# Kernel tuning notes

Hardware: AMD Instinct MI355X
Metric: run time of the kernel (lower is better)

Reference implementation:

```python
import math
import jax, jax.numpy as jnp
import numpy as np

B, T, D, K, R, KC = 4, 2048, 1024, 8, 16, 4
H = 4 * D  # mlp hidden


def setup_inputs() -> dict:
    key = jax.random.key(0)
    ks = jax.random.split(key, 12)
    s = lambda i, shape: jax.random.normal(ks[i], shape, jnp.float32) * 0.02
    # state_decay_logit init: geometric decays in [dmin, dmax], logit = log(p) - log1p(-p)
    dmin, dmax = 0.9, 0.999
    dec = np.exp(np.linspace(math.log(dmin), math.log(dmax), K))
    decay_logit = jnp.asarray(np.log(dec) - np.log1p(-dec), jnp.float32)
    return dict(
        x=jax.random.normal(ks[0], (B, T, D), jnp.float32),
        conv_w=s(1, (D, 1, KC)),            # depthwise conv kernel (torch Conv1d weight)
        gp_w=s(2, (D, D)), gp_b=jnp.zeros((D,), jnp.float32),
        up_w=s(3, (D, H)), up_b=jnp.zeros((H,), jnp.float32),
        dn_w=s(4, (H, D)), dn_b=jnp.zeros((D,), jnp.float32),
        si_w=s(5, (D, K * D)),              # state_in (no bias)
        so_w=s(6, (K * D, D)),              # state_out (no bias)
        decay_logit=decay_logit,
        rs_w=s(7, (D, R)), rs_b=jnp.zeros((R,), jnp.float32),
        rwg_w=s(8, (D, 1)), rwg_b=jnp.zeros((1,), jnp.float32),
        rv_w=s(9, (D, D)), rv_b=jnp.zeros((D,), jnp.float32),
        gr_w=s(10, (D, 1)), gr_b=jnp.zeros((1,), jnp.float32),
        gl_w=s(11, (D, 1)), gl_b=jnp.zeros((1,), jnp.float32),
    )


def _rms_norm(x, eps=1e-6):
    return x * jax.lax.rsqrt(jnp.mean(x * x, axis=-1, keepdims=True) + eps)


def _forward(x, conv_w, gp_w, gp_b, up_w, up_b, dn_w, dn_b, si_w, so_w,
             decay_logit, rs_w, rs_b, rwg_w, rwg_b, rv_w, rv_b, gr_w, gr_b, gl_w, gl_b):
    Bx, Tx, Dx = x.shape
    u = _rms_norm(x)
    # --- local mixer: causal depthwise conv + sigmoid gate + SiLU MLP ---
    xc = jax.lax.conv_general_dilated(
        jnp.swapaxes(u, 1, 2), conv_w, window_strides=(1,),
        padding=[(KC - 1, 0)], feature_group_count=Dx,
        dimension_numbers=('NCH', 'OIH', 'NCH'))
    xc = jnp.swapaxes(xc, 1, 2)                       # (B,T,D) causal conv output
    xg = xc * jax.nn.sigmoid(xc @ gp_w + gp_b)
    local = jax.nn.silu(xg @ up_w + up_b) @ dn_w + dn_b
    # --- per-channel exponential-decay state + register read/write scan ---
    dec = jax.nn.sigmoid(decay_logit)                 # (K,)
    z = (u @ si_w).reshape(Bx, Tx, K, Dx)             # state_in, (B,T,K,D)
    sel = jax.nn.softmax(u @ rs_w + rs_b, axis=-1)    # soft register address (B,T,R)
    wg = jax.nn.sigmoid(u @ rwg_w + rwg_b)            # write gate (B,T,1)
    v = u @ rv_w + rv_b                                # register value (B,T,D)

    def step(carry, inp):
        s, regs = carry
        z_t, sel_t, w_t, v_t = inp
        read = jnp.einsum('br,brd->bd', sel_t, regs)  # soft read before write
        ws = (w_t * sel_t)[:, :, None]                # (B,R,1)
        regs = regs * (1.0 - ws) + ws * v_t[:, None, :]
        s = dec[None, :, None] * s + z_t
        return (s, regs), (s, read)

    init = (jnp.zeros((Bx, K, Dx), x.dtype), jnp.zeros((Bx, R, Dx), x.dtype))
    tm = lambda a: jnp.swapaxes(a, 0, 1)              # time-major for scan
    _, (s_all, reads) = jax.lax.scan(step, init, (tm(z), tm(sel), tm(wg), tm(v)))
    s_all = tm(s_all)                                 # (B,T,K,D)
    reads = tm(reads)                                 # (B,T,D)
    long_out = jnp.einsum('btkd,kde->bte', s_all, so_w.reshape(K, Dx, Dx))
    g_long = jax.nn.sigmoid(u @ gl_w + gl_b)
    g_reg = jax.nn.sigmoid(u @ gr_w + gr_b)
    return x + local + g_long * long_out + g_reg * reads


def reference(x, conv_w, gp_w, gp_b, up_w, up_b, dn_w, dn_b, si_w, so_w,
              decay_logit, rs_w, rs_b, rwg_w, rwg_b, rv_w, rv_b, gr_w, gr_b, gl_w, gl_b):
    return _forward(x, conv_w, gp_w, gp_b, up_w, up_b, dn_w, dn_b, si_w, so_w,
                    decay_logit, rs_w, rs_b, rwg_w, rwg_b, rv_w, rv_b, gr_w, gr_b, gl_w, gl_b)
```

## Files before the change

kernel.cpp:

```cpp
#include <hip/hip_runtime.h>

typedef unsigned short u16;
typedef __bf16 bf16x8 __attribute__((ext_vector_type(8)));
typedef float f32x4 __attribute__((ext_vector_type(4)));
typedef u16 u16x4 __attribute__((ext_vector_type(4)));

#define D_ 1024
#define T_ 2048
#define B_ 4
#define K_ 8
#define R_ 16
#define H_ 4096
#define NROW (B_*T_)
#define CH 32
#define CL (T_/CH)
#define CHS 64
#define CLS (T_/CHS)

__device__ __forceinline__ u16 f2bf(float f){
  union{float f;unsigned u;} v; v.f=f;
  unsigned r = v.u + 0x7FFFu + ((v.u>>16)&1u);
  return (u16)(r>>16);
}
__device__ __forceinline__ float bf2f(u16 b){
  union{unsigned u;float f;} v; v.u = ((unsigned)b)<<16; return v.f;
}
__device__ __forceinline__ float sigm(float x){ return 1.f/(1.f+__expf(-x)); }

__device__ __forceinline__ void gload_lds16(const void* g, void* l){
  __builtin_amdgcn_global_load_lds((const __attribute__((address_space(1))) void*)g,
                                   (__attribute__((address_space(3))) void*)l, 16, 0, 0);
}

__global__ __launch_bounds__(256) void fill_k(float* __restrict__ out, long n, float v){
  long i = (long)blockIdx.x*256 + threadIdx.x;
  if (i < n) out[i] = v;
}

__global__ __launch_bounds__(256) void transpose_cast(const float* __restrict__ in, u16* __restrict__ out,
                                                      int R, int C){
  __shared__ float tile[32][33];
  int bx = blockIdx.x*32;
  int by = blockIdx.y*32;
  int tx = threadIdx.x & 31, ty = threadIdx.x >> 5;
  #pragma unroll
  for (int i=0;i<32;i+=8) tile[ty+i][tx] = in[(size_t)(by+ty+i)*C + bx+tx];
  __syncthreads();
  #pragma unroll
  for (int i=0;i<32;i+=8) out[(size_t)(bx+ty+i)*R + by+tx] = f2bf(tile[tx][ty+i]);
}

__global__ __launch_bounds__(256) void castbf(const float* __restrict__ in, u16* __restrict__ out, long n){
  long i = (long)blockIdx.x*256 + threadIdx.x;
  if (i < n) out[i] = f2bf(in[i]);
}

__global__ __launch_bounds__(256) void initout_k(const float* __restrict__ x, const float* __restrict__ b,
                                                 float* __restrict__ out){
  size_t i = ((size_t)blockIdx.x*256 + threadIdx.x)*4;
  f32x4 xv = *(const f32x4*)(x + i);
  f32x4 bv = *(const f32x4*)(b + (i & (D_-1)));
  xv += bv;
  *(f32x4*)(out + i) = xv;
}

__global__ __launch_bounds__(256) void rmsnorm_k(const float* __restrict__ x, u16* __restrict__ u){
  int row = blockIdx.x;
  const float* xr = x + (size_t)row*D_;
  float xv[4]; float ss = 0.f;
  #pragma unroll
  for (int i=0;i<4;i++){ xv[i] = xr[threadIdx.x + 256*i]; ss += xv[i]*xv[i]; }
  #pragma unroll
  for (int o=32;o>0;o>>=1) ss += __shfl_down(ss, o);
  __shared__ float red[4];
  if ((threadIdx.x&63)==0) red[threadIdx.x>>6] = ss;
  __syncthreads();
  float tot = red[0]+red[1]+red[2]+red[3];
  float r = rsqrtf(tot*(1.f/D_) + 1e-6f);
  #pragma unroll
  for (int i=0;i<4;i++) u[(size_t)row*D_ + threadIdx.x + 256*i] = f2bf(xv[i]*r);
}

__global__ __launch_bounds__(256) void conv_k(const u16* __restrict__ u, const float* __restrict__ w,
                                              u16* __restrict__ xc){
  size_t base = ((size_t)blockIdx.x*256 + threadIdx.x)*4;
  int t  = (int)((base >> 10) & (T_-1));
  int d0 = (int)(base & (D_-1));
  f32x4 wv[4];
  #pragma unroll
  for (int jj=0;jj<4;jj++) wv[jj] = *(const f32x4*)&w[(d0+jj)*4];
  float acc[4] = {0.f,0.f,0.f,0.f};
  #pragma unroll
  for (int j=0;j<4;j++){
    if (t-3+j >= 0){
      u16x4 uv = *(const u16x4*)(u + base + (long)(j-3)*D_);
      #pragma unroll
      for (int jj=0;jj<4;jj++) acc[jj] += bf2f(uv[jj]) * wv[jj][j];
    }
  }
  u16x4 o;
  #pragma unroll
  for (int jj=0;jj<4;jj++) o[jj] = f2bf(acc[jj]);
  *(u16x4*)(xc + base) = o;
}

__global__ __launch_bounds__(256) void smalln_k(const u16* __restrict__ u,
    const float* __restrict__ rs_w, const float* __restrict__ rs_b,
    const float* __restrict__ rwg_w, const float* __restrict__ rwg_b,
    const float* __restrict__ gl_w, const float* __restrict__ gl_b,
    const float* __restrict__ gr_w, const float* __restrict__ gr_b,
    float* __restrict__ sel, float* __restrict__ wg, float* __restrict__ gl, float* __restrict__ gr){
  int row = blockIdx.x, tid = threadIdx.x;
  float p[19];
  #pragma unroll
  for (int c=0;c<19;c++) p[c] = 0.f;
  for (int i=0;i<4;i++){
    int e = tid + i*256;
    float ue = bf2f(u[(size_t)row*D_ + e]);
    const float* rw = rs_w + (size_t)e*16;
    #pragma unroll
    for (int r=0;r<16;r++) p[r] += ue*rw[r];
    p[16] += ue*rwg_w[e];
    p[17] += ue*gl_w[e];
    p[18] += ue*gr_w[e];
  }
  __shared__ float red[19*4];
  #pragma unroll
  for (int c=0;c<19;c++){
    float v = p[c];
    #pragma unroll
    for (int o=32;o>0;o>>=1) v += __shfl_down(v, o);
    if ((tid&63)==0) red[c*4 + (tid>>6)] = v;
  }
  __syncthreads();
  if (tid==0){
    float s[19];
    #pragma unroll
    for (int c=0;c<19;c++) s[c] = red[c*4]+red[c*4+1]+red[c*4+2]+red[c*4+3];
    float mx = -1e30f;
    #pragma unroll
    for (int r=0;r<16;r++){ s[r] += rs_b[r]; mx = fmaxf(mx, s[r]); }
    float ssum = 0.f;
    #pragma unroll
    for (int r=0;r<16;r++){ s[r] = __expf(s[r]-mx); ssum += s[r]; }
    float inv = 1.f/ssum;
    #pragma unroll
    for (int r=0;r<16;r++) sel[(size_t)row*16+r] = s[r]*inv;
    wg[row] = sigm(s[16] + rwg_b[0]);
    gl[row] = sigm(s[17] + gl_b[0]);
    gr[row] = sigm(s[18] + gr_b[0]);
  }
}

#define BM 128
#define BN 128
#define BK 32

template<int EPI>
__global__ __launch_bounds__(256)
void gemm_bt(const u16* __restrict__ A, const u16* __restrict__ BT,
             void* __restrict__ outp, const float* __restrict__ bias,
             const void* __restrict__ aux,
             int K, int lda, int ldb, int ldc,
             long zA, long zB, long zC)
{
  __shared__ __attribute__((aligned(16))) u16 As[BM*BK];
  __shared__ __attribute__((aligned(16))) u16 Bs[BN*BK];
  int nwg = gridDim.x*gridDim.y;
  int bx = blockIdx.x, by = blockIdx.y;
  if ((nwg & 7) == 0){
    int bid = blockIdx.y*gridDim.x + blockIdx.x;
    int cpx = nwg >> 3;
    int s = (bid & 7)*cpx + (bid >> 3);
    bx = s % gridDim.x; by = s / gridDim.x;
  }
  const u16* Ab = A + (size_t)blockIdx.z*zA + (size_t)bx*BM*lda;
  const u16* Bb = BT + (size_t)blockIdx.z*zB + (size_t)by*BN*ldb;
  int tid = threadIdx.x, lane = tid&63, wid = tid>>6;
  int wr = wid>>1, wc = wid&1;
  f32x4 acc[4][4];
  #pragma unroll
  for (int m=0;m<4;m++)
    #pragma unroll
    for (int n=0;n<4;n++) acc[m][n] = (f32x4){0.f,0.f,0.f,0.f};

  int srow = lane>>2;
  int scol = (lane&3)*8;
  int klo  = (lane>>4)*8;
  for (int k0=0; k0<K; k0+=BK){
    #pragma unroll
    for (int i=0;i<2;i++){
      int r0 = wid*32 + i*16;
      gload_lds16(Ab + (size_t)(r0+srow)*lda + k0 + scol, &As[r0*BK]);
      gload_lds16(Bb + (size_t)(r0+srow)*ldb + k0 + scol, &Bs[r0*BK]);
    }
    __syncthreads();
    bf16x8 af[4], bfr[4];
    #pragma unroll
    for (int m=0;m<4;m++) af[m] = *(const bf16x8*)&As[(wr*64+m*16+(lane&15))*BK + klo];
    #pragma unroll
    for (int n=0;n<4;n++) bfr[n] = *(const bf16x8*)&Bs[(wc*64+n*16+(lane&15))*BK + klo];
    #pragma unroll
    for (int m=0;m<4;m++)
      #pragma unroll
      for (int n=0;n<4;n++)
        acc[m][n] = __builtin_amdgcn_mfma_f32_16x16x32_bf16(af[m], bfr[n], acc[m][n], 0, 0, 0);
    __syncthreads();
  }

  size_t obase = (size_t)blockIdx.z*zC;
  int row0 = bx*BM + wr*64;
  int col0 = by*BN + wc*64;
  #pragma unroll
  for (int m=0;m<4;m++){
    #pragma unroll
    for (int n=0;n<4;n++){
      int col = col0 + n*16 + (lane&15);
      #pragma unroll
      for (int r=0;r<4;r++){
        int row = row0 + m*16 + (lane>>4)*4 + r;
        float c = acc[m][n][r];
        size_t idx = obase + (size_t)row*ldc + col;
        if (EPI==0){ ((u16*)outp)[idx] = f2bf(c); }
        else if (EPI==1){ ((u16*)outp)[idx] = f2bf(c + bias[col]); }
        else if (EPI==2){ float t=c+bias[col]; ((u16*)outp)[idx] = f2bf(bf2f(((const u16*)aux)[idx]) * sigm(t)); }
        else if (EPI==3){ float t=c+bias[col]; ((u16*)outp)[idx] = f2bf(t*sigm(t)); }
        else if (EPI==4){ ((float*)outp)[idx] = ((const float*)aux)[idx] + c + bias[col]; }
        else            { ((float*)outp)[idx] += c; }
      }
    }
  }
}

template<int NT, int EPI>
__global__ __launch_bounds__(512, 2)
void gemm8p(const u16* __restrict__ A, const u16* __restrict__ BT,
            void* __restrict__ outp, const float* __restrict__ bias,
            const void* __restrict__ aux,
            int lda, int ldb, int ldc, long zA, long zB, long zC,
            int rx, int ry, int nry)
{
  __shared__ __attribute__((aligned(16))) u16 lds8[65536];
  int bid = blockIdx.y*gridDim.x + blockIdx.x;
  int xcd = bid & 7;
  int s   = bid >> 3;
  int rgx = xcd / nry, rgy = xcd - rgx*nry;
  int bx = rgx*rx + (s % rx);
  int by = rgy*ry + (s / rx);

  const u16* Ab = A + (size_t)blockIdx.z*zA + (size_t)bx*256*lda;
  const u16* Bb = BT + (size_t)blockIdx.z*zB + (size_t)by*256*ldb;

  int tid = threadIdx.x, l = tid&63, w = tid>>6;
  int wr = w>>2, wc = w&3;
  int rS0 = (w*2+0)*8 + (l>>3);
  int rS1 = (w*2+1)*8 + (l>>3);
  int cg  = (((l&7) ^ (l>>3)) << 3);
  int seg0 = (w*2+0)*512;
  int seg1 = (w*2+1)*512;

  auto STAGE = [&](int h){
    int kt = h>>2, idx = h&3, par = kt&1;
    int koff = kt*64;
    if (idx < 2){
      const u16* s0 = Bb + (size_t)(idx*128 + rS0)*ldb + koff + cg;
      const u16* s1 = Bb + (size_t)(idx*128 + rS1)*ldb + koff + cg;
      u16* d = &lds8[par*32768 + 16384 + idx*8192];
      gload_lds16(s0, d + seg0);
      gload_lds16(s1, d + seg1);
    } else {
      int a = idx-2;
      const u16* s0 = Ab + (size_t)(a*128 + rS0)*lda + koff + cg;
      const u16* s1 = Ab + (size_t)(a*128 + rS1)*lda + koff + cg;
      u16* d = &lds8[par*32768 + a*8192];
      gload_lds16(s0, d + seg0);
      gload_lds16(s1, d + seg1);
    }
  };

  f32x4 acc[8][4];
  #pragma unroll
  for (int m=0;m<8;m++)
    #pragma unroll
    for (int n=0;n<4;n++) acc[m][n] = (f32x4){0.f,0.f,0.f,0.f};

  for (int h=0; h<7; ++h) STAGE(h);
  asm volatile("s_waitcnt vmcnt(6)" ::: "memory");
  __builtin_amdgcn_s_barrier();

  for (int it=0; it<NT/2; ++it){
    #pragma unroll
    for (int sub=0; sub<2; ++sub){
      int kt = it*2+sub;
      const int par = sub;
      u16* Abase = &lds8[par*32768 + wr*8192];
      u16* Bbase = &lds8[par*32768 + 16384 + (wc>>1)*8192];
      bf16x8 bf[4][2];
      #pragma unroll
      for (int q=0; q<4; ++q){
        bf16x8 af[2][2];
        if (q==0){
          #pragma unroll
          for (int n=0;n<4;n++)
            #pragma unroll
            for (int ss=0;ss<2;ss++){
              int rr = (wc&1)*64 + n*16 + (l&15);
              int c16 = (l>>4) + ss*4;
              bf[n][ss] = *(const bf16x8*)&Bbase[rr*64 + ((c16 ^ (rr&7))<<3)];
            }
        }
        #pragma unroll
        for (int i=0;i<2;i++)
          #pragma unroll
          for (int ss=0;ss<2;ss++){
            int rr = q*32 + i*16 + (l&15);
            int c16 = (l>>4) + ss*4;
            af[i][ss] = *(const bf16x8*)&Abase[rr*64 + ((c16 ^ (rr&7))<<3)];
          }
        __builtin_amdgcn_sched_barrier(0);
        int h = kt*4 + q + 7;
        if (h < 4*NT) STAGE(h);
        __builtin_amdgcn_s_barrier();
        asm volatile("s_waitcnt lgkmcnt(0)" ::: "memory");
        __builtin_amdgcn_sched_barrier(0);
        __builtin_amdgcn_s_setprio(1);
        #pragma unroll
        for (int i=0;i<2;i++)
          #pragma unroll
          for (int n=0;n<4;n++)
            #pragma unroll
            for (int ss=0;ss<2;ss++)
              acc[q*2+i][n] = __builtin_amdgcn_mfma_f32_16x16x32_bf16(af[i][ss], bf[n][ss], acc[q*2+i][n], 0, 0, 0);
        __builtin_amdgcn_s_setprio(0);
        if (q==3){
          if (kt == NT-2)      asm volatile("s_waitcnt vmcnt(0)" ::: "memory");
          else if (kt < NT-2)  asm volatile("s_waitcnt vmcnt(6)" ::: "memory");
        }
        __builtin_amdgcn_s_barrier();
      }
    }
  }

  size_t obase = (size_t)blockIdx.z*zC;
  int row0 = bx*256 + wr*128;
  int col0 = by*256 + wc*64;
  #pragma unroll
  for (int m=0;m<8;m++){
    #pragma unroll
    for (int n=0;n<4;n++){
      int col = col0 + n*16 + (l&15);
      #pragma unroll
      for (int r=0;r<4;r++){
        int row = row0 + m*16 + (l>>4)*4 + r;
        float c = acc[m][n][r];
        size_t idx = obase + (size_t)row*ldc + col;
        if (EPI==0){ ((u16*)outp)[idx] = f2bf(c); }
        else if (EPI==1){ ((u16*)outp)[idx] = f2bf(c + bias[col]); }
        else if (EPI==2){ float t=c+bias[col]; ((u16*)outp)[idx] = f2bf(bf2f(((const u16*)aux)[idx]) * sigm(t)); }
        else if (EPI==3){ float t=c+bias[col]; ((u16*)outp)[idx] = f2bf(t*sigm(t)); }
        else            { unsafeAtomicAdd(&((float*)outp)[idx], c); }
      }
    }
  }
}

template<int KH>
__global__ __launch_bounds__(256) void scan_s1v(const u16* __restrict__ y, const float* __restrict__ logit,
                                                int p, float* __restrict__ Hend){
  int e0 = threadIdx.x*4;
  int c = blockIdx.y, b = blockIdx.z;
  float dec[KH]; f32x4 h[KH];
  #pragma unroll
  for (int k=0;k<KH;k++){ dec[k] = sigm(logit[KH*p+k]); h[k] = (f32x4){0.f,0.f,0.f,0.f}; }
  size_t row0 = (size_t)b*T_ + (size_t)c*CLS;
  for (int t=0;t<CLS;t++){
    const u16* yp = y + (row0+t)*(size_t)(KH*D_) + e0;
    #pragma unroll
    for (int k=0;k<KH;k++){
      u16x4 w = *(const u16x4*)(yp + (size_t)k*D_);
      #pragma unroll
      for (int j=0;j<4;j++) h[k][j] = dec[k]*h[k][j] + bf2f(w[j]);
    }
  }
  #pragma unroll
  for (int k=0;k<KH;k++)
    *(f32x4*)&Hend[(((size_t)b*CHS+c)*KH+k)*D_ + e0] = h[k];
}

template<int KH>
__global__ __launch_bounds__(256) void scan_s2v(const float* __restrict__ Hend, const float* __restrict__ logit,
                                                int p, float* __restrict__ Sinit){
  int idx = blockIdx.x*256 + threadIdx.x;
  if (idx >= B_*KH*D_) return;
  int e = idx % D_; int kh = (idx/D_) % KH; int b = idx/(D_*KH);
  float dec = sigm(logit[KH*p+kh]);
  float dL = powf(dec, (float)CLS);
  float carry = 0.f;
  for (int c=0;c<CHS;c++){
    size_t i3 = (((size_t)b*CHS+c)*KH+kh)*D_ + e;
    Sinit[i3] = carry;
    carry = dL*carry + Hend[i3];
  }
}

template<int KH>
__global__ __launch_bounds__(256) void scan_s3v(const u16* __restrict__ y, const float* __restrict__ logit,
                                                int p, const float* __restrict__ Sinit,
                                                const float* __restrict__ glb, float* __restrict__ out){
  int e0 = threadIdx.x*4;
  int c = blockIdx.y, b = blockIdx.z;
  float dec[KH]; f32x4 h[KH];
  #pragma unroll
  for (int k=0;k<KH;k++){
    dec[k] = sigm(logit[KH*p+k]);
    h[k] = *(const f32x4*)&Sinit[(((size_t)b*CHS+c)*KH+k)*D_ + e0];
  }
  size_t row0 = (size_t)b*T_ + (size_t)c*CLS;
  for (int t=0;t<CLS;t++){
    const u16* yp = y + (row0+t)*(size_t)(KH*D_) + e0;
    f32x4 sum = (f32x4){0.f,0.f,0.f,0.f};
    #pragma unroll
    for (int k=0;k<KH;k++){
      u16x4 w = *(const u16x4*)(yp + (size_t)k*D_);
      #pragma unroll
      for (int j=0;j<4;j++){ h[k][j] = dec[k]*h[k][j] + bf2f(w[j]); sum[j] += h[k][j]; }
    }
    float g = glb[row0+t];
    f32x4* op = (f32x4*)&out[(row0+t)*D_ + e0];
    f32x4 ov = *op;
    #pragma unroll
    for (int j=0;j<4;j++) ov[j] += g*sum[j];
    *op = ov;
  }
}

__global__ __launch_bounds__(256) void scan_r1(const u16* __restrict__ v, const float* __restrict__ sel,
                                               const float* __restrict__ wg,
                                               float* __restrict__ Rend, float* __restrict__ Pout){
  int d = blockIdx.x*256 + threadIdx.x;
  int c = blockIdx.y, b = blockIdx.z;
  __shared__ float sel_s[CL*R_];
  __shared__ float wg_s[CL];
  size_t row0 = (size_t)b*T_ + (size_t)c*CL;
  for (int i=threadIdx.x; i<CL*R_; i+=256) sel_s[i] = sel[row0*R_ + i];
  for (int i=threadIdx.x; i<CL;    i+=256) wg_s[i]  = wg[row0 + i];
  __syncthreads();
  float regs[R_], P[R_];
  #pragma unroll
  for (int r=0;r<R_;r++){ regs[r]=0.f; P[r]=1.f; }
  for (int t=0;t<CL;t++){
    float vv = bf2f(v[(row0+t)*D_ + d]);
    float w = wg_s[t];
    #pragma unroll
    for (int r=0;r<R_;r++){
      float ws = w*sel_s[t*R_+r];
      regs[r] += ws*(vv - regs[r]);
      P[r] *= (1.f - ws);
    }
  }
  #pragma unroll
  for (int r=0;r<R_;r++) Rend[(((size_t)b*CH+c)*R_+r)*D_ + d] = regs[r];
  if (blockIdx.x==0 && threadIdx.x==0){
    #pragma unroll
    for (int r=0;r<R_;r++) Pout[((size_t)b*CH+c)*R_ + r] = P[r];
  }
}

__global__ __launch_bounds__(256) void scan_r2(const float* __restrict__ Rend, const float* __restrict__ Pbuf,
                                               float* __restrict__ Rinit){
  int idx = blockIdx.x*256 + threadIdx.x;
  if (idx >= B_*D_) return;
  int d = idx % D_; int b = idx / D_;
  float regs[R_];
  #pragma unroll
  for (int r=0;r<R_;r++) regs[r] = 0.f;
  for (int c=0;c<CH;c++){
    #pragma unroll
    for (int r=0;r<R_;r++){
      size_t i3 = (((size_t)b*CH+c)*R_+r)*D_ + d;
      Rinit[i3] = regs[r];
      regs[r] = Pbuf[((size_t)b*CH+c)*R_+r]*regs[r] + Rend[i3];
    }
  }
}

__global__ __launch_bounds__(256) void scan_r3(const u16* __restrict__ v, const float* __restrict__ sel,
                                               const float* __restrict__ wg, const float* __restrict__ Rinit,
                                               const float* __restrict__ grb, float* __restrict__ out){
  int d = blockIdx.x*256 + threadIdx.x;
  int c = blockIdx.y, b = blockIdx.z;
  __shared__ float sel_s[CL*R_];
  __shared__ float wg_s[CL];
  size_t row0 = (size_t)b*T_ + (size_t)c*CL;
  for (int i=threadIdx.x; i<CL*R_; i+=256) sel_s[i] = sel[row0*R_ + i];
  for (int i=threadIdx.x; i<CL;    i+=256) wg_s[i]  = wg[row0 + i];
  __syncthreads();
  float regs[R_];
  #pragma unroll
  for (int r=0;r<R_;r++) regs[r] = Rinit[(((size_t)b*CH+c)*R_+r)*D_ + d];
  for (int t=0;t<CL;t++){
    float vv = bf2f(v[(row0+t)*D_ + d]);
    float w = wg_s[t];
    float read = 0.f;
    #pragma unroll
    for (int r=0;r<R_;r++){
      float sr = sel_s[t*R_+r];
      read += sr*regs[r];
      float ws = w*sr;
      regs[r] += ws*(vv - regs[r]);
    }
    out[(row0+t)*D_ + d] += grb[row0+t]*read;
  }
}

static void launch_gemm(int epi, dim3 g, const u16* A, const u16* BT, void* out,
                        const float* bias, const void* aux, int K, int lda, int ldb, int ldc,
                        long zA, long zB, long zC, hipStream_t s){
  switch(epi){
    case 0: gemm_bt<0><<<g,256,0,s>>>(A,BT,out,bias,aux,K,lda,ldb,ldc,zA,zB,zC); break;
    case 1: gemm_bt<1><<<g,256,0,s>>>(A,BT,out,bias,aux,K,lda,ldb,ldc,zA,zB,zC); break;
    case 2: gemm_bt<2><<<g,256,0,s>>>(A,BT,out,bias,aux,K,lda,ldb,ldc,zA,zB,zC); break;
    case 3: gemm_bt<3><<<g,256,0,s>>>(A,BT,out,bias,aux,K,lda,ldb,ldc,zA,zB,zC); break;
    case 4: gemm_bt<4><<<g,256,0,s>>>(A,BT,out,bias,aux,K,lda,ldb,ldc,zA,zB,zC); break;
    default: gemm_bt<5><<<g,256,0,s>>>(A,BT,out,bias,aux,K,lda,ldb,ldc,zA,zB,zC); break;
  }
}

extern "C" void kernel_launch(void* const* d_in, const int* in_sizes, int n_in,
                              void* d_out, int out_size, void* d_ws, size_t ws_size,
                              hipStream_t stream){
  const float* x      = (const float*)d_in[0];
  const float* conv_w = (const float*)d_in[1];
  const float* gp_w   = (const float*)d_in[2];
  const float* gp_b   = (const float*)d_in[3];
  const float* up_w   = (const float*)d_in[4];
  const float* up_b   = (const float*)d_in[5];
  const float* dn_w   = (const float*)d_in[6];
  const float* dn_b   = (const float*)d_in[7];
  const float* si_w   = (const float*)d_in[8];
  const float* so_w   = (const float*)d_in[9];
  const float* logit  = (const float*)d_in[10];
  const float* rs_w   = (const float*)d_in[11];
  const float* rs_b   = (const float*)d_in[12];
  const float* rwg_w  = (const float*)d_in[13];
  const float* rwg_b  = (const float*)d_in[14];
  const float* rv_w   = (const float*)d_in[15];
  const float* rv_b   = (const float*)d_in[16];
  const float* gr_w   = (const float*)d_in[17];
  const float* gr_b   = (const float*)d_in[18];
  const float* gl_w   = (const float*)d_in[19];
  const float* gl_b   = (const float*)d_in[20];
  float* out = (float*)d_out;
  char* base = (char*)d_ws;

  {
    size_t off = 0;
    auto al = [&](size_t b)->char*{ char* r = base+off; off += (b+255)&~(size_t)255; return r; };
    char* u_r    = al((size_t)NROW*D_*2);
    char* v_r    = al((size_t)NROW*D_*2);
    char* big    = al((size_t)121634816);
    float* sel   = (float*)al((size_t)NROW*R_*4);
    float* wgb   = (float*)al((size_t)NROW*4);
    float* glb   = (float*)al((size_t)NROW*4);
    float* grb   = (float*)al((size_t)NROW*4);
    float* Pbuf  = (float*)al((size_t)B_*CH*R_*4);
    float* Rend  = (float*)al((size_t)B_*CH*R_*D_*4);
    float* Rinit = (float*)al((size_t)B_*CH*R_*D_*4);
    if (off <= ws_size){
      u16* u_bf  = (u16*)u_r;
      u16* v_bf  = (u16*)v_r;
      u16* hid   = (u16*)big;
      u16* xc_bf = (u16*)(big + (size_t)67108864);
      u16* xg_bf = (u16*)(big + (size_t)83886080);
      u16* gpT   = (u16*)(big + (size_t)100663296);
      u16* upT   = (u16*)(big + (size_t)102760448);
      u16* dnT   = (u16*)(big + (size_t)111149056);
      u16* rvT   = (u16*)(big + (size_t)119537664);
      u16* WT    = (u16*)big;
      u16* si_bf = (u16*)(big + (size_t)16777216);
      u16* soT   = (u16*)(big + (size_t)33554432);
      u16* y_bf  = (u16*)(big + (size_t)16777216);
      float* Hend  = (float*)(big + (size_t)83886080);
      float* Sinit = (float*)(big + (size_t)88080384);

      transpose_cast<<<dim3(D_/32, D_/32),256,0,stream>>>(gp_w, gpT, D_, D_);
      transpose_cast<<<dim3(H_/32, D_/32),256,0,stream>>>(up_w, upT, D_, H_);
      transpose_cast<<<dim3(D_/32, H_/32),256,0,stream>>>(dn_w, dnT, H_, D_);
      transpose_cast<<<dim3(D_/32, D_/32),256,0,stream>>>(rv_w, rvT, D_, D_);

      rmsnorm_k<<<NROW,256,0,stream>>>(x, u_bf);
      conv_k<<<(NROW*D_)/1024,256,0,stream>>>(u_bf, conv_w, xc_bf);
      smalln_k<<<NROW,256,0,stream>>>(u_bf, rs_w, rs_b, rwg_w, rwg_b, gl_w, gl_b, gr_w, gr_b,
                                      sel, wgb, glb, grb);

      gemm8p<16,2><<<dim3(NROW/256, D_/256), 512, 0, stream>>>(
          xc_bf, gpT, xg_bf, gp_b, xc_bf, D_, D_, D_, 0, 0, 0, 4, 4, 1);
      gemm8p<16,3><<<dim3(NROW/256, H_/256), 512, 0, stream>>>(
          xg_bf, upT, hid, up_b, nullptr, D_, D_, H_, 0, 0, 0, 8, 8, 2);
      initout_k<<<(NROW*D_)/1024,256,0,stream>>>(x, dn_b, out);
      gemm8p<32,5><<<dim3(NROW/256, D_/256, 2), 512, 0, stream>>>(
          hid, dnT, out, nullptr, nullptr, H_, H_, D_, 2048, 2048, 0, 4, 4, 1);
      gemm8p<16,1><<<dim3(NROW/256, D_/256), 512, 0, stream>>>(
          u_bf, rvT, v_bf, rv_b, nullptr, D_, D_, D_, 0, 0, 0, 4, 4, 1);

      transpose_cast<<<dim3(D_/32, (K_*D_)/32),256,0,stream>>>(so_w, soT, K_*D_, D_);
      castbf<<<((long)D_*K_*D_+255)/256,256,0,stream>>>(si_w, si_bf, (long)D_*K_*D_);
      gemm8p<16,0><<<dim3(D_/256, D_/256, K_), 512, 0, stream>>>(
          soT, si_bf, WT, nullptr, nullptr, K_*D_, K_*D_, D_, (long)D_, (long)D_, (long)D_*D_, 2, 1, 4);

      for (int h=0; h<2; h++){
        gemm8p<16,0><<<dim3(NROW/256, (4*D_)/256), 512, 0, stream>>>(
            u_bf, WT + (size_t)h*4*D_*D_, y_bf, nullptr, nullptr, D_, D_, 4*D_, 0, 0, 0, 8, 8, 2);
        scan_s1v<4><<<dim3(1, CHS, B_),256,0,stream>>>(y_bf, logit, h, Hend);
        scan_s2v<4><<<(B_*4*D_+255)/256,256,0,stream>>>(Hend, logit, h, Sinit);
        scan_s3v<4><<<dim3(1, CHS, B_),256,0,stream>>>(y_bf, logit, h, Sinit, glb, out);
      }

      scan_r1<<<dim3(D_/256, CH, B_),256,0,stream>>>(v_bf, sel, wgb, Rend, Pbuf);
      scan_r2<<<(B_*D_+255)/256,256,0,stream>>>(Rend, Pbuf, Rinit);
      scan_r3<<<dim3(D_/256, CH, B_),256,0,stream>>>(v_bf, sel, wgb, Rinit, grb, out);
      return;
    }
  }

  const size_t MB16_8 = (size_t)NROW*D_*2;
  size_t off = 0;
  auto alloc = [&](size_t bytes)->char*{
    char* r = base + off; off += (bytes + 255) & ~(size_t)255; return r;
  };
  char* R0 = alloc(MB16_8);
  char* R1 = alloc(MB16_8);
  char* R2 = alloc(2*MB16_8);
  char* R3 = alloc((size_t)21*1024*1024);
  float* sel  = (float*)alloc((size_t)NROW*R_*4);
  float* wgb  = (float*)alloc((size_t)NROW*4);
  float* glb  = (float*)alloc((size_t)NROW*4);
  float* grb  = (float*)alloc((size_t)NROW*4);
  float* Pbuf = (float*)alloc((size_t)B_*CH*R_*4);
  float* Hend = (float*)alloc((size_t)B_*CHS*2*D_*4);
  float* Sinit= (float*)alloc((size_t)B_*CHS*2*D_*4);
  if (off > ws_size){
    fill_k<<<((long)out_size+255)/256,256,0,stream>>>(out, out_size, 12345.0f);
    return;
  }

  u16* u_bf  = (u16*)R0;
  u16* v_bf  = (u16*)R1;
  u16* xc_bf = (u16*)R2;
  u16* xg_bf = (u16*)(R2 + MB16_8);
  u16* hid_bf= (u16*)R2;
  u16* soT   = (u16*)R2;
  u16* si_bf = (u16*)(R2 + MB16_8);
  u16* y_bf  = (u16*)R2;
  u16* gpT   = (u16*)R3;
  u16* upT   = (u16*)(R3 + (size_t)2*1024*1024 + 131072);
  u16* dnT   = (u16*)(R3 + (size_t)10*1024*1024 + 655360);
  u16* rvT   = (u16*)(R3 + (size_t)19*1024*1024);
  u16* WT    = (u16*)R3;
  float* Rend = (float*)R3;
  float* Rinit= (float*)(R3 + (size_t)NROW*D_);

  transpose_cast<<<dim3(D_/32, D_/32),256,0,stream>>>(gp_w, gpT, D_, D_);
  transpose_cast<<<dim3(H_/32, D_/32),256,0,stream>>>(up_w, upT, D_, H_);
  transpose_cast<<<dim3(D_/32, H_/32),256,0,stream>>>(dn_w, dnT, H_, D_);
  transpose_cast<<<dim3(D_/32, D_/32),256,0,stream>>>(rv_w, rvT, D_, D_);

  rmsnorm_k<<<NROW,256,0,stream>>>(x, u_bf);
  conv_k<<<(NROW*D_)/1024,256,0,stream>>>(u_bf, conv_w, xc_bf);
  smalln_k<<<NROW,256,0,stream>>>(u_bf, rs_w, rs_b, rwg_w, rwg_b, gl_w, gl_b, gr_w, gr_b,
                                  sel, wgb, glb, grb);

  launch_gemm(2, dim3(NROW/BM, D_/BN, 1), xc_bf, gpT, xg_bf, gp_b, xc_bf,
              D_, D_, D_, D_, 0, 0, 0, stream);
  launch_gemm(1, dim3(NROW/BM, D_/BN, 1), u_bf, rvT, v_bf, rv_b, nullptr,
              D_, D_, D_, D_, 0, 0, 0, stream);
  for (int q=0; q<4; q++){
    launch_gemm(3, dim3(NROW/BM, 1024/BN, 1), xg_bf, upT + (size_t)q*1024*D_, hid_bf,
                up_b + q*1024, nullptr, D_, D_, D_, 1024, 0, 0, 0, stream);
    launch_gemm(q==0?4:5, dim3(NROW/BM, D_/BN, 1), hid_bf, dnT + (size_t)q*1024, out,
                dn_b, x, 1024, 1024, H_, D_, 0, 0, 0, stream);
  }

  transpose_cast<<<dim3(D_/32, (K_*D_)/32),256,0,stream>>>(so_w, soT, K_*D_, D_);
  castbf<<<((long)D_*K_*D_+255)/256,256,0,stream>>>(si_w, si_bf, (long)D_*K_*D_);
  launch_gemm(0, dim3(D_/BM, D_/BN, K_), soT, si_bf, WT, nullptr, nullptr,
              D_, K_*D_, K_*D_, D_, (long)D_, (long)D_, (long)D_*D_, stream);

  for (int p=0; p<4; p++){
    launch_gemm(0, dim3(NROW/BM, (2*D_)/BN, 1), u_bf, WT + (size_t)(2*p)*D_*D_, y_bf,
                nullptr, nullptr, D_, D_, D_, 2*D_, 0, 0, 0, stream);
    scan_s1v<2><<<dim3(1, CHS, B_),256,0,stream>>>(y_bf, logit, p, Hend);
    scan_s2v<2><<<(B_*2*D_+255)/256,256,0,stream>>>(Hend, logit, p, Sinit);
    scan_s3v<2><<<dim3(1, CHS, B_),256,0,stream>>>(y_bf, logit, p, Sinit, glb, out);
  }

  scan_r1<<<dim3(D_/256, CH, B_),256,0,stream>>>(v_bf, sel, wgb, Rend, Pbuf);
  scan_r2<<<(B_*D_+255)/256,256,0,stream>>>(Rend, Pbuf, Rinit);
  scan_r3<<<dim3(D_/256, CH, B_),256,0,stream>>>(v_bf, sel, wgb, Rinit, grb, out);
}
```

Measured before the change: 707.7 us.

## Batch gate and value projections in one z-launch; use double-buffered GEMM for up-proj

Merges the gate-projection GEMM (xc@gp_w, sigmoid-gated epilogue) and the value GEMM (u@rv_w, bias epilogue) into a single launch. blockIdx.z picks the operand set through pointer offsets, and the epilogue branches on z. This doubles the blocks in flight for two small GEMMs and removes one launch. The up-projection GEMM moves to a new kernel with a simpler whole-tile double-buffered LDS pipeline, replacing the finer-grained quarter-tile staging. The pointer-difference z-strides assume all buffers sit in the same allocation, which they do because they are carved from one big buffer.

```diff
diff --git a/kernel.cpp b/kernel.cpp
--- a/kernel.cpp
+++ b/kernel.cpp
@@ -364,6 +364,253 @@
   }
 }
 
+template<int NT>
+__global__ __launch_bounds__(512, 2)
+void gemm8z(const u16* __restrict__ A, const u16* __restrict__ BT,
+            void* __restrict__ outp, const float* __restrict__ bias,
+            const float* __restrict__ bias2, const void* __restrict__ aux,
+            int lda, int ldb, int ldc, long zA, long zB, long zC,
+            int rx, int ry, int nry)
+{
+  __shared__ __attribute__((aligned(16))) u16 lds8[65536];
+  int bid = blockIdx.y*gridDim.x + blockIdx.x;
+  int xcd = bid & 7;
+  int s   = bid >> 3;
+  int rgx = xcd / nry, rgy = xcd - rgx*nry;
+  int bx = rgx*rx + (s % rx);
+  int by = rgy*ry + (s / rx);
+
+  const u16* Ab = A + (size_t)blockIdx.z*zA + (size_t)bx*256*lda;
+  const u16* Bb = BT + (size_t)blockIdx.z*zB + (size_t)by*256*ldb;
+
+  int tid = threadIdx.x, l = tid&63, w = tid>>6;
+  int wr = w>>2, wc = w&3;
+  int rS0 = (w*2+0)*8 + (l>>3);
+  int rS1 = (w*2+1)*8 + (l>>3);
+  int cg  = (((l&7) ^ (l>>3)) << 3);
+  int seg0 = (w*2+0)*512;
+  int seg1 = (w*2+1)*512;
+
+  auto STAGE = [&](int h){
+    int kt = h>>2, idx = h&3, par = kt&1;
+    int koff = kt*64;
+    if (idx < 2){
+      const u16* s0 = Bb + (size_t)(idx*128 + rS0)*ldb + koff + cg;
+      const u16* s1 = Bb + (size_t)(idx*128 + rS1)*ldb + koff + cg;
+      u16* d = &lds8[par*32768 + 16384 + idx*8192];
+      gload_lds16(s0, d + seg0);
+      gload_lds16(s1, d + seg1);
+    } else {
+      int a = idx-2;
+      const u16* s0 = Ab + (size_t)(a*128 + rS0)*lda + koff + cg;
+      const u16* s1 = Ab + (size_t)(a*128 + rS1)*lda + koff + cg;
+      u16* d = &lds8[par*32768 + a*8192];
+      gload_lds16(s0, d + seg0);
+      gload_lds16(s1, d + seg1);
+    }
+  };
+
+  f32x4 acc[8][4];
+  #pragma unroll
+  for (int m=0;m<8;m++)
+    #pragma unroll
+    for (int n=0;n<4;n++) acc[m][n] = (f32x4){0.f,0.f,0.f,0.f};
+
+  for (int h=0; h<7; ++h) STAGE(h);
+  asm volatile("s_waitcnt vmcnt(6)" ::: "memory");
+  __builtin_amdgcn_s_barrier();
+
+  for (int it=0; it<NT/2; ++it){
+    #pragma unroll
+    for (int sub=0; sub<2; ++sub){
+      int kt = it*2+sub;
+      const int par = sub;
+      u16* Abase = &lds8[par*32768 + wr*8192];
+      u16* Bbase = &lds8[par*32768 + 16384 + (wc>>1)*8192];
+      bf16x8 bf[4][2];
+      #pragma unroll
+      for (int q=0; q<4; ++q){
+        bf16x8 af[2][2];
+        if (q==0){
+          #pragma unroll
+          for (int n=0;n<4;n++)
+            #pragma unroll
+            for (int ss=0;ss<2;ss++){
+              int rr = (wc&1)*64 + n*16 + (l&15);
+              int c16 = (l>>4) + ss*4;
+              bf[n][ss] = *(const bf16x8*)&Bbase[rr*64 + ((c16 ^ (rr&7))<<3)];
+            }
+        }
+        #pragma unroll
+        for (int i=0;i<2;i++)
+          #pragma unroll
+          for (int ss=0;ss<2;ss++){
+            int rr = q*32 + i*16 + (l&15);
+            int c16 = (l>>4) + ss*4;
+            af[i][ss] = *(const bf16x8*)&Abase[rr*64 + ((c16 ^ (rr&7))<<3)];
+          }
+        __builtin_amdgcn_sched_barrier(0);
+        int h = kt*4 + q + 7;
+        if (h < 4*NT) STAGE(h);
+        __builtin_amdgcn_s_barrier();
+        asm volatile("s_waitcnt lgkmcnt(0)" ::: "memory");
+        __builtin_amdgcn_sched_barrier(0);
+        __builtin_amdgcn_s_setprio(1);
+        #pragma unroll
+        for (int i=0;i<2;i++)
+          #pragma unroll
+          for (int n=0;n<4;n++)
+            #pragma unroll
+            for (int ss=0;ss<2;ss++)
+              acc[q*2+i][n] = __builtin_amdgcn_mfma_f32_16x16x32_bf16(af[i][ss], bf[n][ss], acc[q*2+i][n], 0, 0, 0);
+        __builtin_amdgcn_s_setprio(0);
+        if (q==3){
+          if (kt == NT-2)      asm volatile("s_waitcnt vmcnt(0)" ::: "memory");
+          else if (kt < NT-2)  asm volatile("s_waitcnt vmcnt(6)" ::: "memory");
+        }
+        __builtin_amdgcn_s_barrier();
+      }
+    }
+  }
+
+  size_t obase = (size_t)blockIdx.z*zC;
+  int row0 = bx*256 + wr*128;
+  int col0 = by*256 + wc*64;
+  bool z0 = (blockIdx.z == 0);
+  #pragma unroll
+  for (int m=0;m<8;m++){
+    #pragma unroll
+    for (int n=0;n<4;n++){
+      int col = col0 + n*16 + (l&15);
+      #pragma unroll
+      for (int r=0;r<4;r++){
+        int row = row0 + m*16 + (l>>4)*4 + r;
+        float c = acc[m][n][r];
+        size_t idx = obase + (size_t)row*ldc + col;
+        if (z0){ float t=c+bias[col]; ((u16*)outp)[idx] = f2bf(bf2f(((const u16*)aux)[idx]) * sigm(t)); }
+        else   { ((u16*)outp)[idx] = f2bf(c + bias2[col]); }
+      }
+    }
+  }
+}
+
+template<int NT, int EPI>
+__global__ __launch_bounds__(512, 2)
+void gemm2p(const u16* __restrict__ A, const u16* __restrict__ BT,
+            void* __restrict__ outp, const float* __restrict__ bias,
+            const void* __restrict__ aux,
+            int lda, int ldb, int ldc, long zA, long zB, long zC,
+            int rx, int ry, int nry)
+{
+  __shared__ __attribute__((aligned(16))) u16 lds8[65536];
+  int bid = blockIdx.y*gridDim.x + blockIdx.x;
+  int xcd = bid & 7;
+  int s   = bid >> 3;
+  int rgx = xcd / nry, rgy = xcd - rgx*nry;
+  int bx = rgx*rx + (s % rx);
+  int by = rgy*ry + (s / rx);
+
+  const u16* Ab = A + (size_t)blockIdx.z*zA + (size_t)bx*256*lda;
+  const u16* Bb = BT + (size_t)blockIdx.z*zB + (size_t)by*256*ldb;
+
+  int tid = threadIdx.x, l = tid&63, w = tid>>6;
+  int wr = w>>2, wc = w&3;
+  int cg  = (((l&7) ^ (l>>3)) << 3);
+  const u16* gA0 = Ab + (size_t)((w*2+0)*8 + (l>>3))*lda + cg;
+  const u16* gA1 = Ab + (size_t)((w*2+1)*8 + (l>>3))*lda + cg;
+  const u16* gB0 = Bb + (size_t)((w*2+0)*8 + (l>>3))*ldb + cg;
+  const u16* gB1 = Bb + (size_t)((w*2+1)*8 + (l>>3))*ldb + cg;
+  size_t a128 = (size_t)128*lda, b128 = (size_t)128*ldb;
+  int seg0 = (w*2+0)*512, seg1 = (w*2+1)*512;
+
+  auto STAGE_TILE = [&](int par){
+    u16* Ad = &lds8[par*32768];
+    u16* Bd = &lds8[par*32768 + 16384];
+    gload_lds16(gB0,        Bd + seg0);
+    gload_lds16(gB1,        Bd + seg1);
+    gload_lds16(gB0 + b128, Bd + 8192 + seg0);
+    gload_lds16(gB1 + b128, Bd + 8192 + seg1);
+    gload_lds16(gA0,        Ad + seg0);
+    gload_lds16(gA1,        Ad + seg1);
+    gload_lds16(gA0 + a128, Ad + 8192 + seg0);
+    gload_lds16(gA1 + a128, Ad + 8192 + seg1);
+    gA0 += 64; gA1 += 64; gB0 += 64; gB1 += 64;
+  };
+
+  f32x4 acc[8][4];
+  #pragma unroll
+  for (int m=0;m<8;m++)
+    #pragma unroll
+    for (int n=0;n<4;n++) acc[m][n] = (f32x4){0.f,0.f,0.f,0.f};
+
+  STAGE_TILE(0);
+  asm volatile("s_waitcnt vmcnt(0)" ::: "memory");
+  __builtin_amdgcn_s_barrier();
+  __builtin_amdgcn_sched_barrier(0);
+
+  for (int kt=0; kt<NT; ++kt){
+    int par = kt&1;
+    if (kt+1 < NT) STAGE_TILE(par^1);
+    u16* Abase = &lds8[par*32768 + wr*8192];
+    u16* Bbase = &lds8[par*32768 + 16384 + (wc>>1)*8192];
+    bf16x8 bf[4][2];
+    #pragma unroll
+    for (int n=0;n<4;n++)
+      #pragma unroll
+      for (int ss=0;ss<2;ss++){
+        int rr = (wc&1)*64 + n*16 + (l&15);
+        int c16 = (l>>4) + ss*4;
+        bf[n][ss] = *(const bf16x8*)&Bbase[rr*64 + ((c16 ^ (rr&7))<<3)];
+      }
+    __builtin_amdgcn_s_setprio(1);
+    #pragma unroll
+    for (int q=0;q<4;q++){
+      bf16x8 af[2][2];
+      #pragma unroll
+      for (int i=0;i<2;i++)
+        #pragma unroll
+        for (int ss=0;ss<2;ss++){
+          int rr = q*32 + i*16 + (l&15);
+          int c16 = (l>>4) + ss*4;
+          af[i][ss] = *(const bf16x8*)&Abase[rr*64 + ((c16 ^ (rr&7))<<3)];
+        }
+      #pragma unroll
+      for (int i=0;i<2;i++)
+        #pragma unroll
+        for (int n=0;n<4;n++)
+          #pragma unroll
+          for (int ss=0;ss<2;ss++)
+            acc[q*2+i][n] = __builtin_amdgcn_mfma_f32_16x16x32_bf16(af[i][ss], bf[n][ss], acc[q*2+i][n], 0, 0, 0);
+    }
+    __builtin_amdgcn_s_setprio(0);
+    asm volatile("s_waitcnt vmcnt(0)" ::: "memory");
+    __builtin_amdgcn_s_barrier();
+    __builtin_amdgcn_sched_barrier(0);
+  }
+
+  size_t obase = (size_t)blockIdx.z*zC;
+  int row0 = bx*256 + wr*128;
+  int col0 = by*256 + wc*64;
+  #pragma unroll
+  for (int m=0;m<8;m++){
+    #pragma unroll
+    for (int n=0;n<4;n++){
+      int col = col0 + n*16 + (l&15);
+      #pragma unroll
+      for (int r=0;r<4;r++){
+        int row = row0 + m*16 + (l>>4)*4 + r;
+        float c = acc[m][n][r];
+        size_t idx = obase + (size_t)row*ldc + col;
+        if (EPI==0){ ((u16*)outp)[idx] = f2bf(c); }
+        else if (EPI==1){ ((u16*)outp)[idx] = f2bf(c + bias[col]); }
+        else if (EPI==2){ float t=c+bias[col]; ((u16*)outp)[idx] = f2bf(bf2f(((const u16*)aux)[idx]) * sigm(t)); }
+        else if (EPI==3){ float t=c+bias[col]; ((u16*)outp)[idx] = f2bf(t*sigm(t)); }
+        else            { unsafeAtomicAdd(&((float*)outp)[idx], c); }
+      }
+    }
+  }
+}
+
 template<int KH>
 __global__ __launch_bounds__(256) void scan_s1v(const u16* __restrict__ y, const float* __restrict__ logit,
                                                 int p, float* __restrict__ Hend){
@@ -593,15 +840,16 @@
       smalln_k<<<NROW,256,0,stream>>>(u_bf, rs_w, rs_b, rwg_w, rwg_b, gl_w, gl_b, gr_w, gr_b,
                                       sel, wgb, glb, grb);
 
-      gemm8p<16,2><<<dim3(NROW/256, D_/256), 512, 0, stream>>>(
-          xc_bf, gpT, xg_bf, gp_b, xc_bf, D_, D_, D_, 0, 0, 0, 4, 4, 1);
-      gemm8p<16,3><<<dim3(NROW/256, H_/256), 512, 0, stream>>>(
+      gemm8z<16><<<dim3(NROW/256, D_/256, 2), 512, 0, stream>>>(
+          xc_bf, gpT, xg_bf, gp_b, rv_b, xc_bf, D_, D_, D_,
+          (long)(u_bf - xc_bf), (long)(rvT - gpT), (long)(v_bf - xg_bf), 4, 4, 1);
+
+      gemm2p<16,3><<<dim3(NROW/256, H_/256), 512, 0, stream>>>(
           xg_bf, upT, hid, up_b, nullptr, D_, D_, H_, 0, 0, 0, 8, 8, 2);
+
       initout_k<<<(NROW*D_)/1024,256,0,stream>>>(x, dn_b, out);
       gemm8p<32,5><<<dim3(NROW/256, D_/256, 2), 512, 0, stream>>>(
           hid, dnT, out, nullptr, nullptr, H_, H_, D_, 2048, 2048, 0, 4, 4, 1);
-      gemm8p<16,1><<<dim3(NROW/256, D_/256), 512, 0, stream>>>(
-          u_bf, rvT, v_bf, rv_b, nullptr, D_, D_, D_, 0, 0, 0, 4, 4, 1);
 
       transpose_cast<<<dim3(D_/32, (K_*D_)/32),256,0,stream>>>(so_w, soT, K_*D_, D_);
       castbf<<<((long)D_*K_*D_+255)/256,256,0,stream>>>(si_w, si_bf, (long)D_*K_*D_);
```

Result: no change. 707.8 us (+0.0%).

## Add 128x128 gemm with XCD-grouped tile remap and batch two D×D GEMMs

Applied to the files above, without the earlier changes.

Adds a new 256-thread 128x128x32 bf16 MFMA GEMM whose block index is remapped so each XCD works on a rectangular region of output tiles. Most GEMM launches (gate, up, down split-K, W precompute, first half of the state projection) switch from the 256x256 gemm8p kernel to it. The gate-projection GEMM and the rv-projection GEMM are merged into one launch via a z-dimension, with a new epilogue that picks per-z behaviour. The aim is better L2 locality and more blocks in flight. The cost is smaller tiles, which means less reuse per loaded tile, and the second state-projection GEMM oddly stays on the old kernel.

```diff
diff --git a/kernel.cpp b/kernel.cpp
--- a/kernel.cpp
+++ b/kernel.cpp
@@ -155,6 +155,93 @@
 #define BM 128
 #define BN 128
 #define BK 32
+
+template<int EPI>
+__global__ __launch_bounds__(256)
+void gemm97(const u16* __restrict__ A, const u16* __restrict__ BT,
+            void* __restrict__ outp, const float* __restrict__ bias,
+            const float* __restrict__ bias2, const void* __restrict__ aux,
+            int K, int lda, int ldb, int ldc,
+            long zA, long zB, long zC,
+            int rx, int ry, int nry)
+{
+  __shared__ __attribute__((aligned(16))) u16 As[BM*BK];
+  __shared__ __attribute__((aligned(16))) u16 Bs[BN*BK];
+  int bid = blockIdx.y*gridDim.x + blockIdx.x;
+  int xcd = bid & 7;
+  int sidx = bid >> 3;
+  int rgx = xcd / nry, rgy = xcd - rgx*nry;
+  int bx = rgx*rx + (sidx % rx);
+  int by = rgy*ry + (sidx / rx);
+  const u16* Ab = A + (size_t)blockIdx.z*zA + (size_t)bx*BM*lda;
+  const u16* Bb = BT + (size_t)blockIdx.z*zB + (size_t)by*BN*ldb;
+  int tid = threadIdx.x, lane = tid&63, wid = tid>>6;
+  int wr = wid>>1, wc = wid&1;
+  f32x4 acc[4][4];
+  #pragma unroll
+  for (int m=0;m<4;m++)
+    #pragma unroll
+    for (int n=0;n<4;n++) acc[m][n] = (f32x4){0.f,0.f,0.f,0.f};
+
+  int srow = lane>>2;
+  int sl   = lane>>4;
+  for (int k0=0; k0<K; k0+=BK){
+    #pragma unroll
+    for (int i=0;i<2;i++){
+      int r0 = wid*32 + i*16;
+      int ra = r0 + srow;
+      int sca = (((lane&3) ^ ((ra>>1)&3)) << 3);
+      gload_lds16(Ab + (size_t)ra*lda + k0 + sca, &As[r0*BK]);
+      gload_lds16(Bb + (size_t)ra*ldb + k0 + sca, &Bs[r0*BK]);
+    }
+    __syncthreads();
+    bf16x8 af[4], bfr[4];
+    #pragma unroll
+    for (int m=0;m<4;m++){
+      int rr = wr*64+m*16+(lane&15);
+      af[m] = *(const bf16x8*)&As[rr*BK + ((sl ^ ((rr>>1)&3))<<3)];
+    }
+    #pragma unroll
+    for (int n=0;n<4;n++){
+      int rr = wc*64+n*16+(lane&15);
+      bfr[n] = *(const bf16x8*)&Bs[rr*BK + ((sl ^ ((rr>>1)&3))<<3)];
+    }
+    #pragma unroll
+    for (int m=0;m<4;m++)
+      #pragma unroll
+      for (int n=0;n<4;n++)
+        acc[m][n] = __builtin_amdgcn_mfma_f32_16x16x32_bf16(af[m], bfr[n], acc[m][n], 0, 0, 0);
+    __syncthreads();
+  }
+
+  size_t obase = (size_t)blockIdx.z*zC;
+  int row0 = bx*BM + wr*64;
+  int col0 = by*BN + wc*64;
+  bool z0 = (blockIdx.z == 0);
+  #pragma unroll
+  for (int m=0;m<4;m++){
+    #pragma unroll
+    for (int n=0;n<4;n++){
+      int col = col0 + n*16 + (lane&15);
+      #pragma unroll
+      for (int r=0;r<4;r++){
+        int row = row0 + m*16 + (lane>>4)*4 + r;
+        float c = acc[m][n][r];
+        size_t idx = obase + (size_t)row*ldc + col;
+        if (EPI==0){ ((u16*)outp)[idx] = f2bf(c); }
+        else if (EPI==1){ ((u16*)outp)[idx] = f2bf(c + bias[col]); }
+        else if (EPI==2){ float t=c+bias[col]; ((u16*)outp)[idx] = f2bf(bf2f(((const u16*)aux)[idx]) * sigm(t)); }
+        else if (EPI==3){ float t=c+bias[col]; ((u16*)outp)[idx] = f2bf(t*sigm(t)); }
+        else if (EPI==4){ ((float*)outp)[idx] = ((const float*)aux)[idx] + c + bias[col]; }
+        else if (EPI==5){ unsafeAtomicAdd(&((float*)outp)[idx], c); }
+        else {
+          if (z0){ float t=c+bias[col]; ((u16*)outp)[idx] = f2bf(bf2f(((const u16*)aux)[idx]) * sigm(t)); }
+          else   { ((u16*)outp)[idx] = f2bf(c + bias2[col]); }
+        }
+      }
+    }
+  }
+}
 
 template<int EPI>
 __global__ __launch_bounds__(256)
@@ -593,22 +680,34 @@
       smalln_k<<<NROW,256,0,stream>>>(u_bf, rs_w, rs_b, rwg_w, rwg_b, gl_w, gl_b, gr_w, gr_b,
                                       sel, wgb, glb, grb);
 
-      gemm8p<16,2><<<dim3(NROW/256, D_/256), 512, 0, stream>>>(
-          xc_bf, gpT, xg_bf, gp_b, xc_bf, D_, D_, D_, 0, 0, 0, 4, 4, 1);
-      gemm8p<16,3><<<dim3(NROW/256, H_/256), 512, 0, stream>>>(
-          xg_bf, upT, hid, up_b, nullptr, D_, D_, H_, 0, 0, 0, 8, 8, 2);
+      gemm97<6><<<dim3(NROW/BM, D_/BN, 2), 256, 0, stream>>>(
+          xc_bf, gpT, xg_bf, gp_b, rv_b, xc_bf, D_, D_, D_, D_,
+          (long)(u_bf - xc_bf), (long)(rvT - gpT), (long)(v_bf - xg_bf), 8, 8, 1);
+
+      gemm97<3><<<dim3(NROW/BM, H_/BN), 256, 0, stream>>>(
+          xg_bf, upT, hid, up_b, nullptr, nullptr, D_, D_, D_, H_, 0, 0, 0, 16, 16, 2);
+
       initout_k<<<(NROW*D_)/1024,256,0,stream>>>(x, dn_b, out);
-      gemm8p<32,5><<<dim3(NROW/256, D_/256, 2), 512, 0, stream>>>(
-          hid, dnT, out, nullptr, nullptr, H_, H_, D_, 2048, 2048, 0, 4, 4, 1);
-      gemm8p<16,1><<<dim3(NROW/256, D_/256), 512, 0, stream>>>(
-          u_bf, rvT, v_bf, rv_b, nullptr, D_, D_, D_, 0, 0, 0, 4, 4, 1);
+      gemm97<5><<<dim3(NROW/BM, D_/BN, 2), 256, 0, stream>>>(
+          hid, dnT, out, nullptr, nullptr, nullptr, 2048, H_, H_, D_, 2048, 2048, 0, 8, 8, 1);
 
       transpose_cast<<<dim3(D_/32, (K_*D_)/32),256,0,stream>>>(so_w, soT, K_*D_, D_);
       castbf<<<((long)D_*K_*D_+255)/256,256,0,stream>>>(si_w, si_bf, (long)D_*K_*D_);
-      gemm8p<16,0><<<dim3(D_/256, D_/256, K_), 512, 0, stream>>>(
-          soT, si_bf, WT, nullptr, nullptr, K_*D_, K_*D_, D_, (long)D_, (long)D_, (long)D_*D_, 2, 1, 4);
-
-      for (int h=0; h<2; h++){
+      gemm97<0><<<dim3(D_/BM, D_/BN, K_), 256, 0, stream>>>(
+          soT, si_bf, WT, nullptr, nullptr, nullptr, D_, K_*D_, K_*D_, D_,
+          (long)D_, (long)D_, (long)D_*D_, 1, 8, 1);
+
+      {
+        int h = 0;
+        gemm97<0><<<dim3(NROW/BM, (4*D_)/BN), 256, 0, stream>>>(
+            u_bf, WT + (size_t)h*4*D_*D_, y_bf, nullptr, nullptr, nullptr,
+            D_, D_, D_, 4*D_, 0, 0, 0, 16, 16, 2);
+        scan_s1v<4><<<dim3(1, CHS, B_),256,0,stream>>>(y_bf, logit, h, Hend);
+        scan_s2v<4><<<(B_*4*D_+255)/256,256,0,stream>>>(Hend, logit, h, Sinit);
+        scan_s3v<4><<<dim3(1, CHS, B_),256,0,stream>>>(y_bf, logit, h, Sinit, glb, out);
+      }
+      {
+        int h = 1;
         gemm8p<16,0><<<dim3(NROW/256, (4*D_)/256), 512, 0, stream>>>(
             u_bf, WT + (size_t)h*4*D_*D_, y_bf, nullptr, nullptr, D_, D_, 4*D_, 0, 0, 0, 8, 8, 2);
         scan_s1v<4><<<dim3(1, CHS, B_),256,0,stream>>>(y_bf, logit, h, Hend);
```

Result: slower. 811.8 us (+14.7%).
